# Kernel tuning notes

Measured on AMD Instinct MI355X. Metric: run time of the kernel, lower is better.

The kernel has to match this reference:

```python
import jax, jax.numpy as jnp
from jax import lax
import numpy as np

B, H, W, C = 2, 128, 128, 256
HEADS, DH = 8, 32
HD = HEADS * DH  # must equal C (pos_emb reshape constraint)


def _lrelu(t):
    return jnp.where(t > 0, t, 0.01 * t)


def _mlp(t, w1, b1, w2):
    # Linear(dim->hd, bias) -> LeakyReLU -> Linear(hd->hd, no bias)
    return _lrelu(t @ w1.T + b1) @ w2.T


def _dwconv(t, w, b):
    # depthwise 3x3, padding 1; t: NCHW, w: (C,1,3,3)
    o = lax.conv_general_dilated(t, w, (1, 1), ((1, 1), (1, 1)),
                                 dimension_numbers=('NCHW', 'OIHW', 'NCHW'),
                                 feature_group_count=t.shape[1])
    return o + b[None, :, None, None]


def setup_inputs():
    key = jax.random.key(0)
    ks = iter(jax.random.split(key, 48))
    def nrm(shape, s=0.02):
        return jax.random.normal(next(ks), shape, jnp.float32) * s
    inp = {
        'x_in': jax.random.normal(next(ks), (B, H, W, C), jnp.float32),
        'y_in': jax.random.normal(next(ks), (B, H, W, C), jnp.float32),
        # fusion_x / fusion_y: two 1x1 convs (stored as (out,in) matrices)
        'fx_w1': nrm((C, 2 * C)), 'fx_b1': jnp.zeros((C,), jnp.float32),
        'fx_w2': nrm((C, C)),     'fx_b2': jnp.zeros((C,), jnp.float32),
        'fy_w1': nrm((C, 2 * C)), 'fy_b1': jnp.zeros((C,), jnp.float32),
        'fy_w2': nrm((C, C)),     'fy_b2': jnp.zeros((C,), jnp.float32),
        # to_q / to_k / to_v: Linear(C->HD,+b) -> LeakyReLU -> Linear(HD->HD, no b)
        'q_w1': nrm((HD, C)), 'q_b1': jnp.zeros((HD,), jnp.float32), 'q_w2': nrm((HD, HD)),
        'k_w1': nrm((HD, C)), 'k_b1': jnp.zeros((HD,), jnp.float32), 'k_w2': nrm((HD, HD)),
        'v_w1': nrm((HD, C)), 'v_b1': jnp.zeros((HD,), jnp.float32), 'v_w2': nrm((HD, HD)),
        'rescale_x': jnp.ones((HEADS, 1, 1), jnp.float32),
        'rescale_y': jnp.ones((HEADS, 1, 1), jnp.float32),
        'px_w': nrm((C, HD)), 'px_b': jnp.zeros((C,), jnp.float32),
        'py_w': nrm((C, HD)), 'py_b': jnp.zeros((C,), jnp.float32),
        # pos_emb: two depthwise 3x3 convs with GELU between
        'pe_w1': nrm((C, 1, 3, 3)), 'pe_b1': jnp.zeros((C,), jnp.float32),
        'pe_w2': nrm((C, 1, 3, 3)), 'pe_b2': jnp.zeros((C,), jnp.float32),
    }
    return inp


def reference(x_in, y_in, fx_w1, fx_b1, fx_w2, fx_b2, fy_w1, fy_b1, fy_w2, fy_b2,
              q_w1, q_b1, q_w2, k_w1, k_b1, k_w2, v_w1, v_b1, v_w2,
              rescale_x, rescale_y, px_w, px_b, py_w, py_b,
              pe_w1, pe_b1, pe_w2, pe_b2):
    b, h, w, c = x_in.shape
    n = h * w

    xy = jnp.concatenate([x_in, y_in], axis=-1)  # (b,h,w,2c)
    fk_x = _lrelu(jnp.einsum('bhwi,oi->bhwo', xy, fx_w1) + fx_b1)
    fk_x = (jnp.einsum('bhwi,oi->bhwo', fk_x, fx_w2) + fx_b2).reshape(b, n, c)
    fk_y = _lrelu(jnp.einsum('bhwi,oi->bhwo', xy, fy_w1) + fy_b1)
    fk_y = (jnp.einsum('bhwi,oi->bhwo', fk_y, fy_w2) + fy_b2).reshape(b, n, c)

    x = x_in.reshape(b, n, c)
    y = y_in.reshape(b, n, c)
    q_inp_x = _mlp(x, q_w1, q_b1, q_w2)
    k_inp_x = _mlp(fk_x, k_w1, k_b1, k_w2)
    v_inp_x = _mlp(x, v_w1, v_b1, v_w2)
    q_inp_y = _mlp(y, q_w1, q_b1, q_w2)
    k_inp_y = _mlp(fk_y, k_w1, k_b1, k_w2)
    v_inp_y = _mlp(y, v_w1, v_b1, v_w2)

    def split_heads(t):  # (b,n,hd) -> (b,heads,d,n)  (already transposed)
        return t.reshape(b, n, HEADS, DH).transpose(0, 2, 3, 1)

    def l2n(t):
        return t / jnp.maximum(jnp.linalg.norm(t, axis=-1, keepdims=True), 1e-12)

    q_x, k_x, v_x = split_heads(q_inp_x), split_heads(k_inp_x), split_heads(v_inp_x)
    q_y, k_y, v_y = split_heads(q_inp_y), split_heads(k_inp_y), split_heads(v_inp_y)
    q_x, k_x, q_y, k_y = l2n(q_x), l2n(k_x), l2n(q_y), l2n(k_y)

    def pos_emb(v_inp):
        t = v_inp.reshape(b, h, w, c).transpose(0, 3, 1, 2)  # NCHW
        t = _dwconv(t, pe_w1, pe_b1)
        t = jax.nn.gelu(t, approximate=False)
        t = _dwconv(t, pe_w2, pe_b2)
        return t.transpose(0, 2, 3, 1)  # NHWC

    # channel (transposed) cross-attention: d x d maps per head
    attn_x = jax.nn.softmax(jnp.einsum('bhdn,bhen->bhde', k_y, q_x) * rescale_x, axis=-1)
    xo = jnp.einsum('bhde,bhen->bhdn', attn_x, v_x).transpose(0, 3, 1, 2).reshape(b, n, HD)
    out_x = (xo @ px_w.T + px_b).reshape(b, h, w, c) + pos_emb(v_inp_x)

    attn_y = jax.nn.softmax(jnp.einsum('bhdn,bhen->bhde', k_x, q_y) * rescale_y, axis=-1)
    yo = jnp.einsum('bhde,bhen->bhdn', attn_y, v_y).transpose(0, 3, 1, 2).reshape(b, n, HD)
    out_y = (yo @ py_w.T + py_b).reshape(b, h, w, c) + pos_emb(v_inp_y)

    return out_x, out_y
```

## Files before the change

### kernel.cpp

```cpp
#include <hip/hip_runtime.h>
#include <hip/hip_bf16.h>

typedef __hip_bfloat16 bf16;
typedef __attribute__((ext_vector_type(8))) short short8;
typedef __attribute__((ext_vector_type(4))) float f32x4;

static __device__ __forceinline__ float bfbits2f(short s) {
    return __uint_as_float(((unsigned int)(unsigned short)s) << 16);
}
static __device__ __forceinline__ float bf2f(bf16 v) { return __bfloat162float(v); }
static __device__ __forceinline__ bf16 f2bf(float v) { return __float2bfloat16(v); }
static __device__ __forceinline__ short f2bfbits(float f) {
    bf16 h = __float2bfloat16(f);
    return *reinterpret_cast<short*>(&h);
}

struct PrepArgs {
    const float *x, *y; bf16 *xb, *yb;
    const float* wsrc[10]; bf16* wdst[10]; int wblk[10];
    const float *pw1, *pw2; float *t1, *t2;
    float4* zero;
};

__launch_bounds__(256)
__global__ void prep_kernel(PrepArgs a)
{
    int blk = blockIdx.x, tid = threadIdx.x;
    if (blk < 8192) {
        int t = blk * 256 + tid;
        int which = t >> 20;
        size_t i = (size_t)(t & 1048575) * 8;
        const float4* s = (const float4*)((which ? a.y : a.x) + i);
        float4 u = s[0], v = s[1];
        short8 p;
        p[0] = f2bfbits(u.x); p[1] = f2bfbits(u.y); p[2] = f2bfbits(u.z); p[3] = f2bfbits(u.w);
        p[4] = f2bfbits(v.x); p[5] = f2bfbits(v.y); p[6] = f2bfbits(v.z); p[7] = f2bfbits(v.w);
        *(short8*)((which ? a.yb : a.xb) + i) = p;
    } else if (blk < 8960) {
        int b = blk - 8192;
        int ai = 0, base = 0;
        while (ai < 9 && b >= base + a.wblk[ai]) { base += a.wblk[ai]; ++ai; }
        size_t i = ((size_t)(b - base) * 256 + tid) * 4;
        const float4 v = *(const float4*)(a.wsrc[ai] + i);
        bf16* d = a.wdst[ai] + i;
        d[0] = f2bf(v.x); d[1] = f2bf(v.y); d[2] = f2bf(v.z); d[3] = f2bf(v.w);
    } else if (blk < 8978) {
        int t = (blk - 8960) * 256 + tid;
        if (t < 4608) {
            int which = t >= 2304;
            int i = which ? t - 2304 : t;
            int c = i / 9, k = i % 9;
            (which ? a.t2 : a.t1)[k * 256 + c] = (which ? a.pw2 : a.pw1)[i];
        }
    } else {
        int i = (blk - 8978) * 256 + tid;
        a.zero[i] = make_float4(0.f, 0.f, 0.f, 0.f);
    }
}

template<int ROWS>
static __device__ __forceinline__ void stage8(const bf16* __restrict__ g, int ldk,
                                              char* dst, int tid, long r0, int k0)
{
#pragma unroll
    for (int r = 0; r < ROWS / 128; ++r) {
        int row = r * 128 + (tid >> 2);
        int q = (tid & 3) * 16;
        int srcq = q ^ (((row >> 1) & 3) << 4);
        const char* gsrc = (const char*)(g + (size_t)(r0 + row) * ldk + k0) + srcq;
        char* ldst = dst + r * 8192 + ((tid >> 6) << 10);
        __builtin_amdgcn_global_load_lds(
            (const __attribute__((address_space(1))) unsigned int*)gsrc,
            (__attribute__((address_space(3))) unsigned int*)ldst, 16, 0, 0);
    }
}

static __device__ __forceinline__ int h_off2(int r, int c)
{
    return r * 512 + ((c * 2) ^ ((r & 7) << 4));
}

struct MlpArgs {
    const bf16* B1[2]; const float* b1[2];
    const bf16* W2[2]; const float* b2[2];
    bf16* outb[2]; bf16* outT[2]; float* nrm[2];
};

template<int K1, bool CONCAT, bool B2OUT, bool TRANS0>
__launch_bounds__(512, 4)
__global__ void mlp_kernel(const bf16* __restrict__ A0, const bf16* __restrict__ A1,
                           MlpArgs args)
{
    __shared__ __align__(16) char lds[66560];
    int tid = threadIdx.x;
    int lane = tid & 63, wid = tid >> 6;
    int c16 = lane & 15, kg = lane >> 4;
    int wr = wid >> 2, wc = wid & 3;
    int sel = blockIdx.x;
    long m0 = (long)blockIdx.y * 128;
    const bf16* B1p = args.B1[sel];
    const bf16* W2p = args.W2[sel];
    char* Abuf = lds;
    char* Bbuf = lds + 16384;

    f32x4 acc[4][4];
#pragma unroll
    for (int i = 0; i < 4; ++i)
#pragma unroll
        for (int j = 0; j < 4; ++j) acc[i][j] = (f32x4){0.f, 0.f, 0.f, 0.f};

    stage8<128>(A0, 256, Abuf, tid, m0, 0);
    stage8<256>(B1p, K1, Bbuf, tid, 0, 0);

    int kb = kg * 16;
    int offa[4], offb[4];
#pragma unroll
    for (int mi = 0; mi < 4; ++mi) {
        int row = wr * 64 + mi * 16 + c16;
        offa[mi] = row * 64 + (kb ^ (((row >> 1) & 3) << 4));
    }
#pragma unroll
    for (int ni = 0; ni < 4; ++ni) {
        int row = wc * 64 + ni * 16 + c16;
        offb[ni] = row * 64 + (kb ^ (((row >> 1) & 3) << 4));
    }

    constexpr int NT1 = K1 / 32;
    for (int kt = 0; kt < NT1; ++kt) {
        __syncthreads();
        int cur = kt & 1;
        if (kt + 1 < NT1) {
            int k0 = (kt + 1) * 32;
            const bf16* As = A0; int kk = k0;
            if (CONCAT && k0 >= 256) { As = A1; kk = k0 - 256; }
            stage8<128>(As, 256, Abuf + (cur ^ 1) * 8192, tid, m0, kk);
            stage8<256>(B1p, K1, Bbuf + (cur ^ 1) * 16384, tid, 0, k0);
        }
        const char* As = Abuf + cur * 8192;
        const char* Bs = Bbuf + cur * 16384;
        short8 af[4], bfr[4];
#pragma unroll
        for (int mi = 0; mi < 4; ++mi) af[mi] = *(const short8*)(As + offa[mi]);
#pragma unroll
        for (int ni = 0; ni < 4; ++ni) bfr[ni] = *(const short8*)(Bs + offb[ni]);
#pragma unroll
        for (int mi = 0; mi < 4; ++mi)
#pragma unroll
            for (int ni = 0; ni < 4; ++ni)
                acc[mi][ni] = __builtin_amdgcn_mfma_f32_16x16x32_bf16(af[mi], bfr[ni], acc[mi][ni], 0, 0, 0);
    }

    int co0 = wid * 32 + c16;
    short8 wf[2][2];
    wf[0][0] = *(const short8*)(W2p + (size_t)co0 * 256 + kg * 8);
    wf[0][1] = *(const short8*)(W2p + (size_t)(co0 + 16) * 256 + kg * 8);

    float bv1[4];
#pragma unroll
    for (int ni = 0; ni < 4; ++ni) bv1[ni] = args.b1[sel][wc * 64 + ni * 16 + c16];
    __syncthreads();
#pragma unroll
    for (int mi = 0; mi < 4; ++mi)
#pragma unroll
        for (int ni = 0; ni < 4; ++ni) {
            int c = wc * 64 + ni * 16 + c16;
#pragma unroll
            for (int j = 0; j < 4; ++j) {
                int r = wr * 64 + mi * 16 + kg * 4 + j;
                float v = acc[mi][ni][j] + bv1[ni];
                v = v > 0.f ? v : 0.01f * v;
                *(bf16*)(lds + h_off2(r, c)) = f2bf(v);
            }
        }
    __syncthreads();

    f32x4 acc2[8][2];
#pragma unroll
    for (int i = 0; i < 8; ++i) {
        acc2[i][0] = (f32x4){0.f, 0.f, 0.f, 0.f};
        acc2[i][1] = (f32x4){0.f, 0.f, 0.f, 0.f};
    }
    for (int kc = 0; kc < 8; ++kc) {
        int cur = kc & 1;
        if (kc < 7) {
            wf[cur ^ 1][0] = *(const short8*)(W2p + (size_t)co0 * 256 + (kc + 1) * 32 + kg * 8);
            wf[cur ^ 1][1] = *(const short8*)(W2p + (size_t)(co0 + 16) * 256 + (kc + 1) * 32 + kg * 8);
        }
#pragma unroll
        for (int mi = 0; mi < 8; ++mi) {
            short8 a2 = *(const short8*)(lds + h_off2(mi * 16 + c16, kc * 32 + kg * 8));
            acc2[mi][0] = __builtin_amdgcn_mfma_f32_16x16x32_bf16(a2, wf[cur][0], acc2[mi][0], 0, 0, 0);
            acc2[mi][1] = __builtin_amdgcn_mfma_f32_16x16x32_bf16(a2, wf[cur][1], acc2[mi][1], 0, 0, 0);
        }
    }

    bool trans = TRANS0 && (sel == 0);
    float vsq[2] = {0.f, 0.f};
    __syncthreads();
    if (trans) {
#pragma unroll
        for (int mi = 0; mi < 8; ++mi)
#pragma unroll
            for (int j2 = 0; j2 < 2; ++j2) {
                int col = co0 + j2 * 16;
#pragma unroll
                for (int j = 0; j < 4; ++j) {
                    float v = acc2[mi][j2][j];
                    vsq[j2] += v * v;
                    int row = mi * 16 + kg * 4 + j;
                    *(bf16*)(lds + col * 256 + ((row * 2) ^ ((col & 7) << 4))) = f2bf(v);
                }
            }
    } else {
        float bvo[2];
        bvo[0] = B2OUT ? args.b2[sel][co0] : 0.f;
        bvo[1] = B2OUT ? args.b2[sel][co0 + 16] : 0.f;
#pragma unroll
        for (int mi = 0; mi < 8; ++mi)
#pragma unroll
            for (int j2 = 0; j2 < 2; ++j2) {
                int col = co0 + j2 * 16;
#pragma unroll
                for (int j = 0; j < 4; ++j) {
                    int row = mi * 16 + kg * 4 + j;
                    *(bf16*)(lds + h_off2(row, col)) = f2bf(acc2[mi][j2][j] + bvo[j2]);
                }
            }
    }
    __syncthreads();
    if (trans) {
        bf16* dst = args.outT[sel];
#pragma unroll
        for (int i = 0; i < 8; ++i) {
            int g = i * 512 + tid;
            int col = g >> 4, rc = g & 15;
            short8 vv = *(const short8*)(lds + col * 256 + ((rc ^ (col & 7)) << 4));
            *(short8*)(dst + (size_t)col * 65536 + m0 + rc * 8) = vv;
        }
        float* cs = (float*)(lds + 65536);
        if (tid < 256) cs[tid] = 0.f;
        __syncthreads();
        atomicAdd(&cs[co0], vsq[0]);
        atomicAdd(&cs[co0 + 16], vsq[1]);
        __syncthreads();
        if (tid < 256)
            atomicAdd(args.nrm[sel] + (int)(m0 >> 14) * 256 + tid, cs[tid]);
    } else {
        bf16* dst = args.outb[sel];
#pragma unroll
        for (int i = 0; i < 8; ++i) {
            int g = i * 512 + tid;
            int row = g >> 5, cc = g & 31;
            short8 vv = *(const short8*)(lds + row * 512 + ((cc ^ (row & 7)) << 4));
            *(short8*)(dst + (size_t)(m0 + row) * 256 + cc * 8) = vv;
        }
    }
}

__launch_bounds__(512, 6)
__global__ void proj_kernel(const bf16* __restrict__ A0, const bf16* __restrict__ Bw,
                            const float* __restrict__ bx, const float* __restrict__ by,
                            float* __restrict__ outf)
{
    __shared__ __align__(16) char lds[49152];
    int tid = threadIdx.x;
    int lane = tid & 63, wid = tid >> 6;
    int c16 = lane & 15, kg = lane >> 4;
    int wr = wid >> 2, wc = wid & 3;
    long m0 = (long)blockIdx.y * 128;
    const bf16* Bp = Bw + (size_t)(m0 >> 14) * 65536;
    char* Abuf = lds;
    char* Bbuf = lds + 16384;

    f32x4 acc[4][4];
#pragma unroll
    for (int i = 0; i < 4; ++i)
#pragma unroll
        for (int j = 0; j < 4; ++j) acc[i][j] = (f32x4){0.f, 0.f, 0.f, 0.f};

    stage8<128>(A0, 256, Abuf, tid, m0, 0);
    stage8<256>(Bp, 256, Bbuf, tid, 0, 0);

    int kb = kg * 16;
    int offa[4], offb[4];
#pragma unroll
    for (int mi = 0; mi < 4; ++mi) {
        int row = wr * 64 + mi * 16 + c16;
        offa[mi] = row * 64 + (kb ^ (((row >> 1) & 3) << 4));
    }
#pragma unroll
    for (int ni = 0; ni < 4; ++ni) {
        int row = wc * 64 + ni * 16 + c16;
        offb[ni] = row * 64 + (kb ^ (((row >> 1) & 3) << 4));
    }

    for (int kt = 0; kt < 8; ++kt) {
        __syncthreads();
        int cur = kt & 1;
        if (kt + 1 < 8) {
            int k0 = (kt + 1) * 32;
            stage8<128>(A0, 256, Abuf + (cur ^ 1) * 8192, tid, m0, k0);
            stage8<256>(Bp, 256, Bbuf + (cur ^ 1) * 16384, tid, 0, k0);
        }
        const char* As = Abuf + cur * 8192;
        const char* Bs = Bbuf + cur * 16384;
        short8 af[4], bfr[4];
#pragma unroll
        for (int mi = 0; mi < 4; ++mi) af[mi] = *(const short8*)(As + offa[mi]);
#pragma unroll
        for (int ni = 0; ni < 4; ++ni) bfr[ni] = *(const short8*)(Bs + offb[ni]);
#pragma unroll
        for (int mi = 0; mi < 4; ++mi)
#pragma unroll
            for (int ni = 0; ni < 4; ++ni)
                acc[mi][ni] = __builtin_amdgcn_mfma_f32_16x16x32_bf16(af[mi], bfr[ni], acc[mi][ni], 0, 0, 0);
    }

    const float* bsel = (m0 >= 32768) ? by : bx;
    float bv[4];
#pragma unroll
    for (int ni = 0; ni < 4; ++ni) bv[ni] = bsel[wc * 64 + ni * 16 + c16];
    long r0 = m0 + wr * 64;
#pragma unroll
    for (int mi = 0; mi < 4; ++mi)
#pragma unroll
        for (int ni = 0; ni < 4; ++ni) {
            int col = wc * 64 + ni * 16 + c16;
#pragma unroll
            for (int j = 0; j < 4; ++j) {
                size_t row = (size_t)(r0 + mi * 16 + kg * 4 + j);
                outf[row * 256 + col] = acc[mi][ni][j] + bv[ni];
            }
        }
}

__launch_bounds__(256)
__global__ void gram_mfma_kernel(const bf16* __restrict__ qT, const bf16* __restrict__ kT,
                                 float* __restrict__ gram)
{
    __shared__ float g[1024];
    int bid = blockIdx.x;
    int ns = bid & 15, h = (bid >> 4) & 7, b = (bid >> 7) & 1, pair = bid >> 8;
    int tid = threadIdx.x;
    int lane = tid & 63, w = tid >> 6;
    long krow = pair ? (long)b * 16384 : (long)(32768 + b * 16384);
    long qrow = pair ? (long)(32768 + b * 16384) : (long)b * 16384;
    long nb = (long)ns * 1024 + w * 256 + (lane >> 4) * 8;
    const bf16* Kp = kT + krow + nb;
    const bf16* Qp = qT + qrow + nb;
    int ch = h * 32 + (lane & 15);

    f32x4 acc[2][2];
#pragma unroll
    for (int i = 0; i < 2; ++i)
#pragma unroll
        for (int j = 0; j < 2; ++j) acc[i][j] = (f32x4){0.f, 0.f, 0.f, 0.f};

    for (int it = 0; it < 8; ++it) {
        short8 af[2], bfr[2];
#pragma unroll
        for (int mi = 0; mi < 2; ++mi)
            af[mi] = *(const short8*)(Kp + (size_t)(ch + mi * 16) * 65536 + it * 32);
#pragma unroll
        for (int ni = 0; ni < 2; ++ni)
            bfr[ni] = *(const short8*)(Qp + (size_t)(ch + ni * 16) * 65536 + it * 32);
#pragma unroll
        for (int mi = 0; mi < 2; ++mi)
#pragma unroll
            for (int ni = 0; ni < 2; ++ni)
                acc[mi][ni] = __builtin_amdgcn_mfma_f32_16x16x32_bf16(af[mi], bfr[ni], acc[mi][ni], 0, 0, 0);
    }

#pragma unroll
    for (int k = 0; k < 4; ++k) g[tid + k * 256] = 0.f;
    __syncthreads();
#pragma unroll
    for (int mi = 0; mi < 2; ++mi)
#pragma unroll
        for (int ni = 0; ni < 2; ++ni) {
            int e = ni * 16 + (lane & 15);
#pragma unroll
            for (int j = 0; j < 4; ++j) {
                int d = mi * 16 + (lane >> 4) * 4 + j;
                atomicAdd(&g[d * 32 + e], acc[mi][ni][j]);
            }
        }
    __syncthreads();
    float* gp = gram + ((size_t)((pair * 2 + b) * 8 + h)) * 1024;
#pragma unroll
    for (int k = 0; k < 4; ++k)
        atomicAdd(gp + tid + k * 256, g[tid + k * 256]);
}

__launch_bounds__(256)
__global__ void attn_pw_kernel(const float* __restrict__ gram, const float* __restrict__ norm2,
                               const float* __restrict__ rsx, const float* __restrict__ rsy,
                               const float* __restrict__ pxw, const float* __restrict__ pyw,
                               bf16* __restrict__ PW)
{
    int bid = blockIdx.x;
    int h = bid & 7, b = (bid >> 3) & 1, pair = bid >> 4;
    const float* G = gram + ((size_t)((pair * 2 + b) * 8 + h)) * 1024;
    const float* nk2 = norm2 + (pair ? (4 + b) : (6 + b)) * 256 + h * 32;
    const float* nq2 = norm2 + (pair ? (2 + b) : (0 + b)) * 256 + h * 32;
    float rs = (pair ? rsy : rsx)[h];
    __shared__ float attn[32][32];
    int t = threadIdx.x;
    if (t < 32) {
        int d = t;
        float nk = fmaxf(sqrtf(nk2[d]), 1e-12f);
        float row[32];
        float mx = -3.4e38f;
#pragma unroll
        for (int e = 0; e < 32; ++e) {
            float nq = fmaxf(sqrtf(nq2[e]), 1e-12f);
            float L = G[d * 32 + e] / (nk * nq) * rs;
            row[e] = L;
            mx = fmaxf(mx, L);
        }
        float sum = 0.f;
#pragma unroll
        for (int e = 0; e < 32; ++e) { row[e] = expf(row[e] - mx); sum += row[e]; }
        float inv = 1.0f / sum;
#pragma unroll
        for (int e = 0; e < 32; ++e) attn[d][e] = row[e] * inv;
    }
    __syncthreads();
    const float* pw = pair ? pyw : pxw;
    int o = t;
    float wrow[32];
#pragma unroll
    for (int d2 = 0; d2 < 32; ++d2) wrow[d2] = pw[o * 256 + h * 32 + d2];
    bf16* dst = PW + ((size_t)(pair * 2 + b) * 256 + o) * 256 + h * 32;
#pragma unroll
    for (int e = 0; e < 32; ++e) {
        float sv = 0.f;
#pragma unroll
        for (int d2 = 0; d2 < 32; ++d2) sv += wrow[d2] * attn[d2][e];
        dst[e] = f2bf(sv);
    }
}

template<bool GELU_OUT_BF>
__launch_bounds__(256)
__global__ void dwconv_kernel(const bf16* __restrict__ in0, const bf16* __restrict__ in1,
                              const float* __restrict__ wT, const float* __restrict__ bias,
                              bf16* __restrict__ ob0, bf16* __restrict__ ob1,
                              float* __restrict__ of0, float* __restrict__ of1)
{
    int blk = blockIdx.x;
    int sel = blk >> 10;
    const bf16* in = sel ? in1 : in0;
    bf16* outb = sel ? ob1 : ob0;
    float* outf = sel ? of1 : of0;
    int t = (blk & 1023) * 256 + threadIdx.x;
    int cg = t & 31;
    int x = (t >> 5) & 127;
    int chunk = (t >> 12) & 31;
    int b = t >> 17;
    int c0 = cg * 8;

    float w[9][8];
#pragma unroll
    for (int k = 0; k < 9; ++k) {
        float4 a = *(const float4*)(wT + k * 256 + c0);
        float4 bq = *(const float4*)(wT + k * 256 + c0 + 4);
        w[k][0] = a.x; w[k][1] = a.y; w[k][2] = a.z; w[k][3] = a.w;
        w[k][4] = bq.x; w[k][5] = bq.y; w[k][6] = bq.z; w[k][7] = bq.w;
    }
    float bs[8];
    {
        float4 a = *(const float4*)(bias + c0);
        float4 bq = *(const float4*)(bias + c0 + 4);
        bs[0] = a.x; bs[1] = a.y; bs[2] = a.z; bs[3] = a.w;
        bs[4] = bq.x; bs[5] = bq.y; bs[6] = bq.z; bs[7] = bq.w;
    }
    const short8 z = (short8){0, 0, 0, 0, 0, 0, 0, 0};
    bool xm = x > 0, xp = x < 127;
    int y0 = chunk * 4;

    for (int yi = 0; yi < 4; ++yi) {
        int y = y0 + yi;
        float acc[8];
#pragma unroll
        for (int j = 0; j < 8; ++j) acc[j] = bs[j];
#pragma unroll
        for (int ky = -1; ky <= 1; ++ky) {
            int yy = y + ky;
            if (yy < 0 || yy > 127) continue;
            const bf16* rp = in + ((((size_t)b << 14) + (yy << 7) + x) << 8) + c0;
            short8 vm = xm ? *(const short8*)(rp - 256) : z;
            short8 vc = *(const short8*)(rp);
            short8 vp = xp ? *(const short8*)(rp + 256) : z;
            int k0 = (ky + 1) * 3;
#pragma unroll
            for (int j = 0; j < 8; ++j) {
                acc[j] += w[k0 + 0][j] * bfbits2f(vm[j]);
                acc[j] += w[k0 + 1][j] * bfbits2f(vc[j]);
                acc[j] += w[k0 + 2][j] * bfbits2f(vp[j]);
            }
        }
        size_t base = ((((size_t)b << 14) + (y << 7) + x) << 8) + c0;
        if (GELU_OUT_BF) {
            short8 p;
#pragma unroll
            for (int j = 0; j < 8; ++j) {
                float a = acc[j];
                a = 0.5f * a * (1.0f + erff(a * 0.70710678118654752f));
                p[j] = f2bfbits(a);
            }
            *(short8*)(outb + base) = p;
        } else {
            float4* o = (float4*)(outf + base);
            float4 o0 = o[0], o1 = o[1];
            o0.x += acc[0]; o0.y += acc[1]; o0.z += acc[2]; o0.w += acc[3];
            o1.x += acc[4]; o1.y += acc[5]; o1.z += acc[6]; o1.w += acc[7];
            o[0] = o0; o[1] = o1;
        }
    }
}

extern "C" void kernel_launch(void* const* d_in, const int* in_sizes, int n_in,
                              void* d_out, int out_size, void* d_ws, size_t ws_size,
                              hipStream_t stream)
{
    const float* x_in  = (const float*)d_in[0];
    const float* y_in  = (const float*)d_in[1];
    const float* fx_w1 = (const float*)d_in[2];
    const float* fx_b1 = (const float*)d_in[3];
    const float* fx_w2 = (const float*)d_in[4];
    const float* fx_b2 = (const float*)d_in[5];
    const float* fy_w1 = (const float*)d_in[6];
    const float* fy_b1 = (const float*)d_in[7];
    const float* fy_w2 = (const float*)d_in[8];
    const float* fy_b2 = (const float*)d_in[9];
    const float* q_w1  = (const float*)d_in[10];
    const float* q_b1  = (const float*)d_in[11];
    const float* q_w2  = (const float*)d_in[12];
    const float* k_w1  = (const float*)d_in[13];
    const float* k_b1  = (const float*)d_in[14];
    const float* k_w2  = (const float*)d_in[15];
    const float* v_w1  = (const float*)d_in[16];
    const float* v_b1  = (const float*)d_in[17];
    const float* v_w2  = (const float*)d_in[18];
    const float* rescale_x = (const float*)d_in[19];
    const float* rescale_y = (const float*)d_in[20];
    const float* px_w  = (const float*)d_in[21];
    const float* px_b  = (const float*)d_in[22];
    const float* py_w  = (const float*)d_in[23];
    const float* py_b  = (const float*)d_in[24];
    const float* pe_w1 = (const float*)d_in[25];
    const float* pe_b1 = (const float*)d_in[26];
    const float* pe_w2 = (const float*)d_in[27];
    const float* pe_b2 = (const float*)d_in[28];

    char* ws = (char*)d_ws;
    const size_t NB = 16777216;
    bf16* xbf  = (bf16*)(ws + 0 * NB);
    bf16* ybf  = (bf16*)(ws + 1 * NB);
    bf16* fkx  = (bf16*)(ws + 2 * NB);
    bf16* fky  = (bf16*)(ws + 3 * NB);
    bf16* vbuf = (bf16*)(ws + 4 * NB);
    bf16* qT   = (bf16*)(ws + 6 * NB);
    bf16* kT   = (bf16*)(ws + 8 * NB);
    char* wreg = ws + 10 * NB;
    bf16* w_fx1 = (bf16*)(wreg + 0);
    bf16* w_fx2 = (bf16*)(wreg + 262144);
    bf16* w_fy1 = (bf16*)(wreg + 393216);
    bf16* w_fy2 = (bf16*)(wreg + 655360);
    bf16* w_q1  = (bf16*)(wreg + 786432);
    bf16* w_q2  = (bf16*)(wreg + 917504);
    bf16* w_k1  = (bf16*)(wreg + 1048576);
    bf16* w_k2  = (bf16*)(wreg + 1179648);
    bf16* w_v1  = (bf16*)(wreg + 1310720);
    bf16* w_v2  = (bf16*)(wreg + 1441792);
    float* gram  = (float*)(wreg + 1572864);
    float* norm2 = (float*)(wreg + 1572864 + 131072);
    bf16* PW     = (bf16*)(wreg + 1572864 + 139264);
    float* peT1  = (float*)(wreg + 1572864 + 139264 + 524288);
    float* peT2  = (float*)(wreg + 1572864 + 139264 + 524288 + 9216);
    bf16* ctmp1  = (bf16*)(ws + 2 * NB);
    bf16* ctmp2  = (bf16*)(ws + 3 * NB);

    float* outx = (float*)d_out;
    float* outy = outx + 8388608;

    PrepArgs pa;
    pa.x = x_in; pa.y = y_in; pa.xb = xbf; pa.yb = ybf;
    const float* ws_src[10] = {fx_w1, fx_w2, fy_w1, fy_w2, q_w1, q_w2, k_w1, k_w2, v_w1, v_w2};
    bf16* ws_dst[10] = {w_fx1, w_fx2, w_fy1, w_fy2, w_q1, w_q2, w_k1, w_k2, w_v1, w_v2};
    int nblk[10] = {128, 64, 128, 64, 64, 64, 64, 64, 64, 64};
    for (int i = 0; i < 10; ++i) { pa.wsrc[i] = ws_src[i]; pa.wdst[i] = ws_dst[i]; pa.wblk[i] = nblk[i]; }
    pa.pw1 = pe_w1; pa.pw2 = pe_w2; pa.t1 = peT1; pa.t2 = peT2;
    pa.zero = (float4*)gram;
    prep_kernel<<<9012, 256, 0, stream>>>(pa);

    MlpArgs fa = {};
    fa.B1[0] = w_fx1; fa.B1[1] = w_fy1; fa.b1[0] = fx_b1; fa.b1[1] = fy_b1;
    fa.W2[0] = w_fx2; fa.W2[1] = w_fy2; fa.b2[0] = fx_b2; fa.b2[1] = fy_b2;
    fa.outb[0] = fkx; fa.outb[1] = fky;
    mlp_kernel<512, true, true, false><<<dim3(2, 256), 512, 0, stream>>>(xbf, ybf, fa);

    MlpArgs qa = {};
    qa.B1[0] = w_q1; qa.B1[1] = w_v1; qa.b1[0] = q_b1; qa.b1[1] = v_b1;
    qa.W2[0] = w_q2; qa.W2[1] = w_v2;
    qa.outT[0] = qT; qa.nrm[0] = norm2;
    qa.outb[1] = vbuf;
    mlp_kernel<256, false, false, true><<<dim3(2, 512), 512, 0, stream>>>(xbf, nullptr, qa);

    MlpArgs ka = {};
    ka.B1[0] = w_k1; ka.b1[0] = k_b1; ka.W2[0] = w_k2;
    ka.outT[0] = kT; ka.nrm[0] = norm2 + 1024;
    mlp_kernel<256, false, false, true><<<dim3(1, 512), 512, 0, stream>>>(fkx, nullptr, ka);

    dwconv_kernel<true><<<2048, 256, 0, stream>>>(vbuf, vbuf + (size_t)32768 * 256,
                                                  peT1, pe_b1, ctmp1, ctmp2, nullptr, nullptr);

    gram_mfma_kernel<<<512, 256, 0, stream>>>(qT, kT, gram);
    attn_pw_kernel<<<32, 256, 0, stream>>>(gram, norm2, rescale_x, rescale_y, px_w, py_w, PW);

    proj_kernel<<<dim3(1, 512), 512, 0, stream>>>(vbuf, PW, px_b, py_b, outx);

    dwconv_kernel<false><<<2048, 256, 0, stream>>>(ctmp1, ctmp2, peT2, pe_b2,
                                                   nullptr, nullptr, outx, outy);
}
```

Baseline: 443.8 us.

## Fuse projection with second dwconv, merge q/v/k MLPs, load B fragments directly

```diff
diff --git a/kernel.cpp b/kernel.cpp
--- a/kernel.cpp
+++ b/kernel.cpp
@@ -8,7 +8,6 @@
 static __device__ __forceinline__ float bfbits2f(short s) {
     return __uint_as_float(((unsigned int)(unsigned short)s) << 16);
 }
-static __device__ __forceinline__ float bf2f(bf16 v) { return __bfloat162float(v); }
 static __device__ __forceinline__ bf16 f2bf(float v) { return __float2bfloat16(v); }
 static __device__ __forceinline__ short f2bfbits(float f) {
     bf16 h = __float2bfloat16(f);
@@ -58,21 +57,17 @@
     }
 }
 
-template<int ROWS>
-static __device__ __forceinline__ void stage8(const bf16* __restrict__ g, int ldk,
+static __device__ __forceinline__ void stageA(const bf16* __restrict__ g,
                                               char* dst, int tid, long r0, int k0)
 {
-#pragma unroll
-    for (int r = 0; r < ROWS / 128; ++r) {
-        int row = r * 128 + (tid >> 2);
-        int q = (tid & 3) * 16;
-        int srcq = q ^ (((row >> 1) & 3) << 4);
-        const char* gsrc = (const char*)(g + (size_t)(r0 + row) * ldk + k0) + srcq;
-        char* ldst = dst + r * 8192 + ((tid >> 6) << 10);
-        __builtin_amdgcn_global_load_lds(
-            (const __attribute__((address_space(1))) unsigned int*)gsrc,
-            (__attribute__((address_space(3))) unsigned int*)ldst, 16, 0, 0);
-    }
+    int row = tid >> 2;
+    int q = (tid & 3) * 16;
+    int srcq = q ^ (((row >> 1) & 3) << 4);
+    const char* gsrc = (const char*)(g + (size_t)(r0 + row) * 256 + k0) + srcq;
+    char* ldst = dst + ((tid >> 6) << 10);
+    __builtin_amdgcn_global_load_lds(
+        (const __attribute__((address_space(1))) unsigned int*)gsrc,
+        (__attribute__((address_space(3))) unsigned int*)ldst, 16, 0, 0);
 }
 
 static __device__ __forceinline__ int h_off2(int r, int c)
@@ -81,15 +76,15 @@
 }
 
 struct MlpArgs {
-    const bf16* B1[2]; const float* b1[2];
-    const bf16* W2[2]; const float* b2[2];
-    bf16* outb[2]; bf16* outT[2]; float* nrm[2];
+    const bf16* A0[3];
+    const bf16* B1[3]; const float* b1[3];
+    const bf16* W2[3]; const float* b2[3];
+    bf16* outb[3]; bf16* outT[3]; float* nrm[3];
 };
 
-template<int K1, bool CONCAT, bool B2OUT, bool TRANS0>
-__launch_bounds__(512, 4)
-__global__ void mlp_kernel(const bf16* __restrict__ A0, const bf16* __restrict__ A1,
-                           MlpArgs args)
+template<int K1, bool CONCAT>
+__launch_bounds__(512, 2)
+__global__ void mlp_kernel(const bf16* __restrict__ A1c, MlpArgs args)
 {
     __shared__ __align__(16) char lds[66560];
     int tid = threadIdx.x;
@@ -98,10 +93,10 @@
     int wr = wid >> 2, wc = wid & 3;
     int sel = blockIdx.x;
     long m0 = (long)blockIdx.y * 128;
+    const bf16* A0 = args.A0[sel];
     const bf16* B1p = args.B1[sel];
     const bf16* W2p = args.W2[sel];
     char* Abuf = lds;
-    char* Bbuf = lds + 16384;
 
     f32x4 acc[4][4];
 #pragma unroll
@@ -109,45 +104,47 @@
 #pragma unroll
         for (int j = 0; j < 4; ++j) acc[i][j] = (f32x4){0.f, 0.f, 0.f, 0.f};
 
-    stage8<128>(A0, 256, Abuf, tid, m0, 0);
-    stage8<256>(B1p, K1, Bbuf, tid, 0, 0);
+    const bf16* brow[4];
+#pragma unroll
+    for (int ni = 0; ni < 4; ++ni)
+        brow[ni] = B1p + (size_t)(wc * 64 + ni * 16 + c16) * K1 + kg * 8;
+
+    stageA(A0, Abuf, tid, m0, 0);
 
     int kb = kg * 16;
-    int offa[4], offb[4];
+    int offa[4];
 #pragma unroll
     for (int mi = 0; mi < 4; ++mi) {
         int row = wr * 64 + mi * 16 + c16;
         offa[mi] = row * 64 + (kb ^ (((row >> 1) & 3) << 4));
     }
-#pragma unroll
-    for (int ni = 0; ni < 4; ++ni) {
-        int row = wc * 64 + ni * 16 + c16;
-        offb[ni] = row * 64 + (kb ^ (((row >> 1) & 3) << 4));
-    }
+
+    short8 bfrag[2][4];
+#pragma unroll
+    for (int ni = 0; ni < 4; ++ni) bfrag[0][ni] = *(const short8*)(brow[ni]);
 
     constexpr int NT1 = K1 / 32;
+#pragma unroll
     for (int kt = 0; kt < NT1; ++kt) {
         __syncthreads();
-        int cur = kt & 1;
         if (kt + 1 < NT1) {
             int k0 = (kt + 1) * 32;
             const bf16* As = A0; int kk = k0;
-            if (CONCAT && k0 >= 256) { As = A1; kk = k0 - 256; }
-            stage8<128>(As, 256, Abuf + (cur ^ 1) * 8192, tid, m0, kk);
-            stage8<256>(B1p, K1, Bbuf + (cur ^ 1) * 16384, tid, 0, k0);
-        }
-        const char* As = Abuf + cur * 8192;
-        const char* Bs = Bbuf + cur * 16384;
-        short8 af[4], bfr[4];
+            if (CONCAT && k0 >= 256) { As = A1c; kk = k0 - 256; }
+            stageA(As, Abuf + ((kt & 1) ^ 1) * 8192, tid, m0, kk);
+#pragma unroll
+            for (int ni = 0; ni < 4; ++ni)
+                bfrag[(kt + 1) & 1][ni] = *(const short8*)(brow[ni] + (kt + 1) * 32);
+        }
+        const char* As = Abuf + (kt & 1) * 8192;
+        short8 af[4];
 #pragma unroll
         for (int mi = 0; mi < 4; ++mi) af[mi] = *(const short8*)(As + offa[mi]);
 #pragma unroll
-        for (int ni = 0; ni < 4; ++ni) bfr[ni] = *(const short8*)(Bs + offb[ni]);
-#pragma unroll
         for (int mi = 0; mi < 4; ++mi)
 #pragma unroll
             for (int ni = 0; ni < 4; ++ni)
-                acc[mi][ni] = __builtin_amdgcn_mfma_f32_16x16x32_bf16(af[mi], bfr[ni], acc[mi][ni], 0, 0, 0);
+                acc[mi][ni] = __builtin_amdgcn_mfma_f32_16x16x32_bf16(af[mi], bfrag[kt & 1][ni], acc[mi][ni], 0, 0, 0);
     }
 
     int co0 = wid * 32 + c16;
@@ -180,21 +177,22 @@
         acc2[i][0] = (f32x4){0.f, 0.f, 0.f, 0.f};
         acc2[i][1] = (f32x4){0.f, 0.f, 0.f, 0.f};
     }
+#pragma unroll
     for (int kc = 0; kc < 8; ++kc) {
-        int cur = kc & 1;
         if (kc < 7) {
-            wf[cur ^ 1][0] = *(const short8*)(W2p + (size_t)co0 * 256 + (kc + 1) * 32 + kg * 8);
-            wf[cur ^ 1][1] = *(const short8*)(W2p + (size_t)(co0 + 16) * 256 + (kc + 1) * 32 + kg * 8);
+            wf[(kc + 1) & 1][0] = *(const short8*)(W2p + (size_t)co0 * 256 + (kc + 1) * 32 + kg * 8);
+            wf[(kc + 1) & 1][1] = *(const short8*)(W2p + (size_t)(co0 + 16) * 256 + (kc + 1) * 32 + kg * 8);
         }
 #pragma unroll
         for (int mi = 0; mi < 8; ++mi) {
             short8 a2 = *(const short8*)(lds + h_off2(mi * 16 + c16, kc * 32 + kg * 8));
-            acc2[mi][0] = __builtin_amdgcn_mfma_f32_16x16x32_bf16(a2, wf[cur][0], acc2[mi][0], 0, 0, 0);
-            acc2[mi][1] = __builtin_amdgcn_mfma_f32_16x16x32_bf16(a2, wf[cur][1], acc2[mi][1], 0, 0, 0);
-        }
-    }
-
-    bool trans = TRANS0 && (sel == 0);
+            acc2[mi][0] = __builtin_amdgcn_mfma_f32_16x16x32_bf16(a2, wf[kc & 1][0], acc2[mi][0], 0, 0, 0);
+            acc2[mi][1] = __builtin_amdgcn_mfma_f32_16x16x32_bf16(a2, wf[kc & 1][1], acc2[mi][1], 0, 0, 0);
+        }
+    }
+
+    bool trans = args.outT[sel] != nullptr;
+    const float* b2p = args.b2[sel];
     float vsq[2] = {0.f, 0.f};
     __syncthreads();
     if (trans) {
@@ -213,8 +211,8 @@
             }
     } else {
         float bvo[2];
-        bvo[0] = B2OUT ? args.b2[sel][co0] : 0.f;
-        bvo[1] = B2OUT ? args.b2[sel][co0 + 16] : 0.f;
+        bvo[0] = b2p ? b2p[co0] : 0.f;
+        bvo[1] = b2p ? b2p[co0 + 16] : 0.f;
 #pragma unroll
         for (int mi = 0; mi < 8; ++mi)
 #pragma unroll
@@ -257,20 +255,25 @@
     }
 }
 
-__launch_bounds__(512, 6)
-__global__ void proj_kernel(const bf16* __restrict__ A0, const bf16* __restrict__ Bw,
-                            const float* __restrict__ bx, const float* __restrict__ by,
-                            float* __restrict__ outf)
-{
-    __shared__ __align__(16) char lds[49152];
+__launch_bounds__(512, 2)
+__global__ void projconv_kernel(const bf16* __restrict__ vbuf, const bf16* __restrict__ PW,
+                                const bf16* __restrict__ ctmp,
+                                const float* __restrict__ px_b, const float* __restrict__ py_b,
+                                const float* __restrict__ peT2, const float* __restrict__ pe_b2,
+                                float* __restrict__ outf)
+{
+    __shared__ __align__(16) char lds[76800];
+    float* ldsF = (float*)lds;
+    float* ldsW = (float*)(lds + 66560);
+    float* ldsB = (float*)(lds + 75776);
     int tid = threadIdx.x;
     int lane = tid & 63, wid = tid >> 6;
     int c16 = lane & 15, kg = lane >> 4;
     int wr = wid >> 2, wc = wid & 3;
     long m0 = (long)blockIdx.y * 128;
-    const bf16* Bp = Bw + (size_t)(m0 >> 14) * 65536;
+    int quarter = (int)(m0 >> 14);
+    int y = (int)((m0 & 16383) >> 7);
     char* Abuf = lds;
-    char* Bbuf = lds + 16384;
 
     f32x4 acc[4][4];
 #pragma unroll
@@ -278,60 +281,101 @@
 #pragma unroll
         for (int j = 0; j < 4; ++j) acc[i][j] = (f32x4){0.f, 0.f, 0.f, 0.f};
 
-    stage8<128>(A0, 256, Abuf, tid, m0, 0);
-    stage8<256>(Bp, 256, Bbuf, tid, 0, 0);
+    const bf16* Bq = PW + (size_t)quarter * 65536;
+    const bf16* brow[4];
+#pragma unroll
+    for (int ni = 0; ni < 4; ++ni)
+        brow[ni] = Bq + (size_t)(wc * 64 + ni * 16 + c16) * 256 + kg * 8;
+
+    stageA(vbuf, Abuf, tid, m0, 0);
+
+#pragma unroll
+    for (int i = 0; i < 5; ++i) {
+        int idx = i * 512 + tid;
+        if (idx < 2304) ldsW[idx] = peT2[idx];
+    }
+    if (tid < 256) ldsB[tid] = (quarter < 2 ? px_b : py_b)[tid] + pe_b2[tid];
 
     int kb = kg * 16;
-    int offa[4], offb[4];
+    int offa[4];
 #pragma unroll
     for (int mi = 0; mi < 4; ++mi) {
         int row = wr * 64 + mi * 16 + c16;
         offa[mi] = row * 64 + (kb ^ (((row >> 1) & 3) << 4));
     }
-#pragma unroll
-    for (int ni = 0; ni < 4; ++ni) {
-        int row = wc * 64 + ni * 16 + c16;
-        offb[ni] = row * 64 + (kb ^ (((row >> 1) & 3) << 4));
-    }
-
+
+    short8 bfrag[2][4];
+#pragma unroll
+    for (int ni = 0; ni < 4; ++ni) bfrag[0][ni] = *(const short8*)(brow[ni]);
+
+#pragma unroll
     for (int kt = 0; kt < 8; ++kt) {
         __syncthreads();
-        int cur = kt & 1;
         if (kt + 1 < 8) {
-            int k0 = (kt + 1) * 32;
-            stage8<128>(A0, 256, Abuf + (cur ^ 1) * 8192, tid, m0, k0);
-            stage8<256>(Bp, 256, Bbuf + (cur ^ 1) * 16384, tid, 0, k0);
-        }
-        const char* As = Abuf + cur * 8192;
-        const char* Bs = Bbuf + cur * 16384;
-        short8 af[4], bfr[4];
+            stageA(vbuf, Abuf + ((kt & 1) ^ 1) * 8192, tid, m0, (kt + 1) * 32);
+#pragma unroll
+            for (int ni = 0; ni < 4; ++ni)
+                bfrag[(kt + 1) & 1][ni] = *(const short8*)(brow[ni] + (kt + 1) * 32);
+        }
+        const char* As = Abuf + (kt & 1) * 8192;
+        short8 af[4];
 #pragma unroll
         for (int mi = 0; mi < 4; ++mi) af[mi] = *(const short8*)(As + offa[mi]);
 #pragma unroll
-        for (int ni = 0; ni < 4; ++ni) bfr[ni] = *(const short8*)(Bs + offb[ni]);
-#pragma unroll
         for (int mi = 0; mi < 4; ++mi)
 #pragma unroll
             for (int ni = 0; ni < 4; ++ni)
-                acc[mi][ni] = __builtin_amdgcn_mfma_f32_16x16x32_bf16(af[mi], bfr[ni], acc[mi][ni], 0, 0, 0);
-    }
-
-    const float* bsel = (m0 >= 32768) ? by : bx;
-    float bv[4];
-#pragma unroll
-    for (int ni = 0; ni < 4; ++ni) bv[ni] = bsel[wc * 64 + ni * 16 + c16];
-    long r0 = m0 + wr * 64;
-#pragma unroll
-    for (int mi = 0; mi < 4; ++mi)
-#pragma unroll
-        for (int ni = 0; ni < 4; ++ni) {
-            int col = wc * 64 + ni * 16 + c16;
-#pragma unroll
-            for (int j = 0; j < 4; ++j) {
-                size_t row = (size_t)(r0 + mi * 16 + kg * 4 + j);
-                outf[row * 256 + col] = acc[mi][ni][j] + bv[ni];
+                acc[mi][ni] = __builtin_amdgcn_mfma_f32_16x16x32_bf16(af[mi], bfrag[kt & 1][ni], acc[mi][ni], 0, 0, 0);
+    }
+
+    const bf16* cbase = ctmp + (((size_t)quarter << 14) << 8);
+#pragma unroll
+    for (int hh = 0; hh < 2; ++hh) {
+        __syncthreads();
+        if (wr == hh) {
+#pragma unroll
+            for (int mi = 0; mi < 4; ++mi)
+#pragma unroll
+                for (int ni = 0; ni < 4; ++ni) {
+                    int col = wc * 64 + ni * 16 + c16;
+#pragma unroll
+                    for (int j = 0; j < 4; ++j)
+                        ldsF[(mi * 16 + kg * 4 + j) * 260 + col] = acc[mi][ni][j];
+                }
+        }
+        __syncthreads();
+#pragma unroll
+        for (int pass = 0; pass < 4; ++pass) {
+            int idx = pass * 512 + tid;
+            int cg = idx & 31, c0 = cg * 8;
+            int xl = idx >> 5;
+            int x = hh * 64 + xl;
+            float a8[8];
+#pragma unroll
+            for (int j = 0; j < 8; ++j) a8[j] = ldsB[c0 + j];
+#pragma unroll
+            for (int dy = -1; dy <= 1; ++dy) {
+                int yy = y + dy;
+                if (yy < 0 || yy > 127) continue;
+#pragma unroll
+                for (int dx = -1; dx <= 1; ++dx) {
+                    int xx = x + dx;
+                    if (xx < 0 || xx > 127) continue;
+                    short8 v = *(const short8*)(cbase + (size_t)((yy << 7) + xx) * 256 + c0);
+                    const float* wt = ldsW + ((dy + 1) * 3 + dx + 1) * 256 + c0;
+#pragma unroll
+                    for (int j = 0; j < 8; ++j) a8[j] += wt[j] * bfbits2f(v[j]);
+                }
             }
-        }
+            const float* pf = ldsF + xl * 260 + c0;
+#pragma unroll
+            for (int j = 0; j < 8; ++j) a8[j] += pf[j];
+            float4 o0 = make_float4(a8[0], a8[1], a8[2], a8[3]);
+            float4 o1 = make_float4(a8[4], a8[5], a8[6], a8[7]);
+            float4* op = (float4*)(outf + (size_t)(m0 + x) * 256 + c0);
+            op[0] = o0; op[1] = o1;
+        }
+    }
 }
 
 __launch_bounds__(256)
@@ -441,23 +485,15 @@
     }
 }
 
-template<bool GELU_OUT_BF>
 __launch_bounds__(256)
-__global__ void dwconv_kernel(const bf16* __restrict__ in0, const bf16* __restrict__ in1,
-                              const float* __restrict__ wT, const float* __restrict__ bias,
-                              bf16* __restrict__ ob0, bf16* __restrict__ ob1,
-                              float* __restrict__ of0, float* __restrict__ of1)
-{
-    int blk = blockIdx.x;
-    int sel = blk >> 10;
-    const bf16* in = sel ? in1 : in0;
-    bf16* outb = sel ? ob1 : ob0;
-    float* outf = sel ? of1 : of0;
-    int t = (blk & 1023) * 256 + threadIdx.x;
+__global__ void dwconv1_kernel(const bf16* __restrict__ in, const float* __restrict__ wT,
+                               const float* __restrict__ bias, bf16* __restrict__ outb)
+{
+    int t = blockIdx.x * 256 + threadIdx.x;
     int cg = t & 31;
     int x = (t >> 5) & 127;
     int chunk = (t >> 12) & 31;
-    int b = t >> 17;
+    int img = t >> 17;
     int c0 = cg * 8;
 
     float w[9][8];
@@ -488,7 +524,7 @@
         for (int ky = -1; ky <= 1; ++ky) {
             int yy = y + ky;
             if (yy < 0 || yy > 127) continue;
-            const bf16* rp = in + ((((size_t)b << 14) + (yy << 7) + x) << 8) + c0;
+            const bf16* rp = in + ((((size_t)img << 14) + (yy << 7) + x) << 8) + c0;
             short8 vm = xm ? *(const short8*)(rp - 256) : z;
             short8 vc = *(const short8*)(rp);
             short8 vp = xp ? *(const short8*)(rp + 256) : z;
@@ -500,23 +536,15 @@
                 acc[j] += w[k0 + 2][j] * bfbits2f(vp[j]);
             }
         }
-        size_t base = ((((size_t)b << 14) + (y << 7) + x) << 8) + c0;
-        if (GELU_OUT_BF) {
-            short8 p;
-#pragma unroll
-            for (int j = 0; j < 8; ++j) {
-                float a = acc[j];
-                a = 0.5f * a * (1.0f + erff(a * 0.70710678118654752f));
-                p[j] = f2bfbits(a);
-            }
-            *(short8*)(outb + base) = p;
-        } else {
-            float4* o = (float4*)(outf + base);
-            float4 o0 = o[0], o1 = o[1];
-            o0.x += acc[0]; o0.y += acc[1]; o0.z += acc[2]; o0.w += acc[3];
-            o1.x += acc[4]; o1.y += acc[5]; o1.z += acc[6]; o1.w += acc[7];
-            o[0] = o0; o[1] = o1;
-        }
+        size_t base = ((((size_t)img << 14) + (y << 7) + x) << 8) + c0;
+        short8 p;
+#pragma unroll
+        for (int j = 0; j < 8; ++j) {
+            float a = acc[j];
+            a = 0.5f * a * (1.0f + erff(a * 0.70710678118654752f));
+            p[j] = f2bfbits(a);
+        }
+        *(short8*)(outb + base) = p;
     }
 }
 
@@ -579,11 +607,9 @@
     bf16* PW     = (bf16*)(wreg + 1572864 + 139264);
     float* peT1  = (float*)(wreg + 1572864 + 139264 + 524288);
     float* peT2  = (float*)(wreg + 1572864 + 139264 + 524288 + 9216);
-    bf16* ctmp1  = (bf16*)(ws + 2 * NB);
-    bf16* ctmp2  = (bf16*)(ws + 3 * NB);
+    bf16* ctmp   = fkx;
 
     float* outx = (float*)d_out;
-    float* outy = outx + 8388608;
 
     PrepArgs pa;
     pa.x = x_in; pa.y = y_in; pa.xb = xbf; pa.yb = ybf;
@@ -596,31 +622,27 @@
     prep_kernel<<<9012, 256, 0, stream>>>(pa);
 
     MlpArgs fa = {};
+    fa.A0[0] = xbf; fa.A0[1] = xbf;
     fa.B1[0] = w_fx1; fa.B1[1] = w_fy1; fa.b1[0] = fx_b1; fa.b1[1] = fy_b1;
     fa.W2[0] = w_fx2; fa.W2[1] = w_fy2; fa.b2[0] = fx_b2; fa.b2[1] = fy_b2;
     fa.outb[0] = fkx; fa.outb[1] = fky;
-    mlp_kernel<512, true, true, false><<<dim3(2, 256), 512, 0, stream>>>(xbf, ybf, fa);
+    mlp_kernel<512, true><<<dim3(2, 256), 512, 0, stream>>>(ybf, fa);
 
     MlpArgs qa = {};
-    qa.B1[0] = w_q1; qa.B1[1] = w_v1; qa.b1[0] = q_b1; qa.b1[1] = v_b1;
-    qa.W2[0] = w_q2; qa.W2[1] = w_v2;
+    qa.A0[0] = xbf; qa.A0[1] = xbf; qa.A0[2] = fkx;
+    qa.B1[0] = w_q1; qa.B1[1] = w_v1; qa.B1[2] = w_k1;
+    qa.b1[0] = q_b1; qa.b1[1] = v_b1; qa.b1[2] = k_b1;
+    qa.W2[0] = w_q2; qa.W2[1] = w_v2; qa.W2[2] = w_k2;
     qa.outT[0] = qT; qa.nrm[0] = norm2;
     qa.outb[1] = vbuf;
-    mlp_kernel<256, false, false, true><<<dim3(2, 512), 512, 0, stream>>>(xbf, nullptr, qa);
-
-    MlpArgs ka = {};
-    ka.B1[0] = w_k1; ka.b1[0] = k_b1; ka.W2[0] = w_k2;
-    ka.outT[0] = kT; ka.nrm[0] = norm2 + 1024;
-    mlp_kernel<256, false, false, true><<<dim3(1, 512), 512, 0, stream>>>(fkx, nullptr, ka);
-
-    dwconv_kernel<true><<<2048, 256, 0, stream>>>(vbuf, vbuf + (size_t)32768 * 256,
-                                                  peT1, pe_b1, ctmp1, ctmp2, nullptr, nullptr);
+    qa.outT[2] = kT; qa.nrm[2] = norm2 + 1024;
+    mlp_kernel<256, false><<<dim3(3, 512), 512, 0, stream>>>(nullptr, qa);
+
+    dwconv1_kernel<<<2048, 256, 0, stream>>>(vbuf, peT1, pe_b1, ctmp);
 
     gram_mfma_kernel<<<512, 256, 0, stream>>>(qT, kT, gram);
     attn_pw_kernel<<<32, 256, 0, stream>>>(gram, norm2, rescale_x, rescale_y, px_w, py_w, PW);
 
-    proj_kernel<<<dim3(1, 512), 512, 0, stream>>>(vbuf, PW, px_b, py_b, outx);
-
-    dwconv_kernel<false><<<2048, 256, 0, stream>>>(ctmp1, ctmp2, peT2, pe_b2,
-                                                   nullptr, nullptr, outx, outy);
-}
+    projconv_kernel<<<dim3(1, 512), 512, 0, stream>>>(vbuf, PW, ctmp, px_b, py_b,
+                                                      peT2, pe_b2, outx);
+}
```

Measured after the change: 524.2 us. +18.1%, slower.
